# Performance work log

Hardware: AMD Instinct MI355X
Metric: run time of the kernel (lower is better)

The kernel has to match this reference:

```python
import jax, jax.numpy as jnp
import numpy as np

N_NODES = 50000
N_EDGES = 600000
D_IN = 128
D_HID = 128
N_CLASS = 40


def gcn_conv(x, edge_index, W, b, num_nodes):
    """PyG GCNConv: add self-loops, symmetric normalization, weight-then-propagate."""
    row, col = edge_index[0], edge_index[1]
    loop = jnp.arange(num_nodes)
    row = jnp.concatenate([row, loop])
    col = jnp.concatenate([col, loop])
    ew = jnp.ones(row.shape[0], dtype=x.dtype)
    deg = jax.ops.segment_sum(ew, col, num_segments=num_nodes)  # in-degree incl. self-loop
    dinv = jnp.where(deg > 0, jax.lax.rsqrt(deg), jnp.zeros((), x.dtype))
    norm = dinv[row] * dinv[col]  # [E+N]
    xw = x @ W  # [N, D]
    msg = norm[:, None] * xw[row]  # gather + scale, [E+N, D]
    out = jax.ops.segment_sum(msg, col, num_segments=num_nodes)  # scatter-add
    return out + b


def setup_inputs() -> dict:
    key = jax.random.key(0)
    ks = jax.random.split(key, 8)
    s_in = 1.0 / np.sqrt(D_IN)
    s_hid = 1.0 / np.sqrt(D_HID)
    return {
        "x": jax.random.normal(ks[0], (N_NODES, D_IN), jnp.float32),
        "edge_index": jax.random.randint(ks[1], (2, N_EDGES), 0, N_NODES, dtype=jnp.int64),
        "W_in": jax.random.normal(ks[2], (D_IN, D_HID), jnp.float32) * s_in,
        "b_in": jnp.zeros((D_HID,), jnp.float32),
        "W_gcn": jax.random.normal(ks[3], (D_HID, D_HID), jnp.float32) * s_hid,
        "b_gcn": jnp.zeros((D_HID,), jnp.float32),
        "W_cls": jax.random.normal(ks[4], (D_HID, N_CLASS), jnp.float32) * s_hid,
        "b_cls": jnp.zeros((N_CLASS,), jnp.float32),
    }


def reference(x, edge_index, W_in, b_in, W_gcn, b_gcn, W_cls, b_cls):
    h = jax.nn.relu(x @ W_in + b_in)               # linear_transform_in
    g = gcn_conv(h, edge_index, W_gcn, b_gcn, N_NODES)  # GCNConv
    y_hat = jax.nn.relu(g) @ W_cls + b_cls          # linear_cls_out
    return y_hat
```

## Files before the change

kernel.cpp:

```cpp
#include <hip/hip_runtime.h>


typedef __bf16 bf16x8 __attribute__((ext_vector_type(8)));
typedef float f32x4 __attribute__((ext_vector_type(4)));

#define NBUCK 512
#define CH_MAX 4704
#define PREP_BLKS 152

__device__ __forceinline__ ushort f2b(float f) {
  uint u = __float_as_uint(f);
  return (ushort)((u + 0x7FFFu + ((u >> 16) & 1u)) >> 16);
}
__device__ __forceinline__ float b2f_lo(uint u) { return __uint_as_float(u << 16); }
__device__ __forceinline__ float b2f_hi(uint u) { return __uint_as_float(u & 0xFFFF0000u); }

__device__ __forceinline__ void acc8s(float* a, uint4 v, float d) {
  a[0] = fmaf(d, b2f_lo(v.x), a[0]); a[1] = fmaf(d, b2f_hi(v.x), a[1]);
  a[2] = fmaf(d, b2f_lo(v.y), a[2]); a[3] = fmaf(d, b2f_hi(v.y), a[3]);
  a[4] = fmaf(d, b2f_lo(v.z), a[4]); a[5] = fmaf(d, b2f_hi(v.z), a[5]);
  a[6] = fmaf(d, b2f_lo(v.w), a[6]); a[7] = fmaf(d, b2f_hi(v.w), a[7]);
}

__global__ __launch_bounds__(256) void k_prep_chist(const float* __restrict__ Wi,
                                                    const float* __restrict__ Wg,
                                                    const float* __restrict__ Wc,
                                                    ushort* __restrict__ Ti,
                                                    ushort* __restrict__ Tg,
                                                    ushort* __restrict__ Tc,
                                                    const int* __restrict__ col,
                                                    int* __restrict__ H2,
                                                    int E, int chunk, int sortb) {
  __shared__ int hist[NBUCK];
  const int tid = threadIdx.x;
  if (blockIdx.x < PREP_BLKS) {
    int idx = blockIdx.x * 256 + tid;
    if (idx < 16384) {
      int c = idx >> 7, k = idx & 127;
      Ti[c * 128 + k] = f2b(Wi[k * 128 + c]);
    } else if (idx < 32768) {
      int j = idx - 16384;
      int c = j >> 7, k = j & 127;
      Tg[c * 128 + k] = f2b(Wg[k * 128 + c]);
    } else if (idx < 38912) {
      int j = idx - 32768;
      int c = j >> 7, k = j & 127;
      Tc[c * 128 + k] = (c < 40) ? f2b(Wc[k * 40 + c]) : (ushort)0;
    }
    return;
  }
  const int blk = blockIdx.x - PREP_BLKS;
  for (int b = tid; b < NBUCK; b += 256) hist[b] = 0;
  __syncthreads();
  const int e0 = blk * chunk;
  const int cnt = min(chunk, E - e0);
  for (int i = tid; i < cnt; i += 256)
    atomicAdd(&hist[((unsigned)col[e0 + i]) >> 7], 1);
  __syncthreads();
  for (int b = tid; b < NBUCK; b += 256)
    H2[b * sortb + blk] = hist[b];
}

__global__ __launch_bounds__(512) void k_scan_gemm1(const int* __restrict__ H2,
                                                    int* __restrict__ Hs,
                                                    int* __restrict__ cursor,
                                                    int sortb,
                                                    const float* __restrict__ x,
                                                    const ushort* __restrict__ Wti,
                                                    const float* __restrict__ b_in,
                                                    ushort* __restrict__ h, int nrows) {
  __shared__ __align__(16) char smem[69632];
  const int tid = threadIdx.x;
  if (blockIdx.x == 0) {
    int* sd = (int*)smem;
    int s = 0;
    const int4* p = (const int4*)&H2[tid * sortb];
    for (int j = 0; j < sortb / 4; ++j) { int4 v = p[j]; s += v.x + v.y + v.z + v.w; }
    sd[tid] = s;
    __syncthreads();
    for (int off = 1; off < 512; off <<= 1) {
      int u = (tid >= off) ? sd[tid - off] : 0;
      __syncthreads();
      sd[tid] += u;
      __syncthreads();
    }
    Hs[tid] = sd[tid] - s;
    if (tid == 511) Hs[NBUCK] = sd[511];
    cursor[tid] = 0;
    return;
  }
  ushort (*As)[136] = (ushort(*)[136])smem;
  ushort (*Bs)[136] = (ushort(*)[136])(smem + 128 * 136 * 2);
  const int row0 = (blockIdx.x - 1) * 128;
#pragma unroll
  for (int q = 0; q < 4; ++q) {
    int f = tid + 512 * q;
    int r = f >> 4, cw = f & 15;
    *(uint4*)&Bs[r][cw * 8] = *(const uint4*)&Wti[r * 128 + cw * 8];
  }
#pragma unroll
  for (int q = 0; q < 8; ++q) {
    int f = tid + 512 * q;
    int r = f >> 5, kc = f & 31;
    float4 v = make_float4(0.f, 0.f, 0.f, 0.f);
    if (row0 + r < nrows) v = *(const float4*)&x[(size_t)(row0 + r) * 128 + kc * 4];
    ushort4 o;
    o.x = f2b(v.x); o.y = f2b(v.y); o.z = f2b(v.z); o.w = f2b(v.w);
    *(ushort4*)&As[r][kc * 4] = o;
  }
  __syncthreads();

  const int wid = tid >> 6, lane = tid & 63;
  const int fr = lane & 15, fg = lane >> 4;
  f32x4 acc[8];
#pragma unroll
  for (int n = 0; n < 8; ++n) acc[n] = (f32x4){0.f, 0.f, 0.f, 0.f};
#pragma unroll
  for (int ks = 0; ks < 4; ++ks) {
    const int kb = ks * 32 + fg * 8;
    bf16x8 a = *(const bf16x8*)&As[wid * 16 + fr][kb];
#pragma unroll
    for (int n = 0; n < 8; ++n) {
      bf16x8 b = *(const bf16x8*)&Bs[n * 16 + fr][kb];
      acc[n] = __builtin_amdgcn_mfma_f32_16x16x32_bf16(a, b, acc[n], 0, 0, 0);
    }
  }
  const int r0 = row0 + wid * 16 + fg * 4;
#pragma unroll
  for (int n = 0; n < 8; ++n) {
    const int cn = n * 16 + fr;
    const float bv = b_in[cn];
#pragma unroll
    for (int i = 0; i < 4; ++i) {
      const int rr = r0 + i;
      if (rr < nrows) h[(size_t)rr * 128 + cn] = f2b(fmaxf(acc[n][i] + bv, 0.f));
    }
  }
}

__global__ __launch_bounds__(256) void k_reorder_gemm2(const int* __restrict__ row,
                                                       const int* __restrict__ col,
                                                       const int* __restrict__ Hs,
                                                       int* __restrict__ cursor,
                                                       uint* __restrict__ ebuf,
                                                       int E, int chunk, int sortb,
                                                       const ushort* __restrict__ h,
                                                       const ushort* __restrict__ Wtg,
                                                       ushort* __restrict__ xws,
                                                       int nrows) {
  __shared__ __align__(16) char smem[52224];
  const int tid = threadIdx.x;
  if (blockIdx.x < sortb) {
    int* hist   = (int*)smem;
    int* lstart = hist + NBUCK;
    int* cnt2   = lstart + NBUCK;
    int* obase  = cnt2 + NBUCK;
    uint* data  = (uint*)(obase + NBUCK);
    int* gpos   = (int*)(data + CH_MAX);
    int* sd     = gpos + CH_MAX;
    for (int b = tid; b < NBUCK; b += 256) { hist[b] = 0; cnt2[b] = 0; }
    __syncthreads();
    const int e0 = blockIdx.x * chunk;
    const int cnt = min(chunk, E - e0);
    for (int i = tid; i < cnt; i += 256)
      atomicAdd(&hist[((unsigned)col[e0 + i]) >> 7], 1);
    __syncthreads();
    const int h0 = hist[2 * tid], h1 = hist[2 * tid + 1];
    const int ps = h0 + h1;
    sd[tid] = ps;
    __syncthreads();
    for (int off = 1; off < 256; off <<= 1) {
      int u = (tid >= off) ? sd[tid - off] : 0;
      __syncthreads();
      sd[tid] += u;
      __syncthreads();
    }
    const int ex = sd[tid] - ps;
    lstart[2 * tid] = ex;
    lstart[2 * tid + 1] = ex + h0;
    obase[2 * tid]     = Hs[2 * tid]     + (h0 ? atomicAdd(&cursor[2 * tid], h0) : 0);
    obase[2 * tid + 1] = Hs[2 * tid + 1] + (h1 ? atomicAdd(&cursor[2 * tid + 1], h1) : 0);
    __syncthreads();
    for (int i = tid; i < cnt; i += 256) {
      const int c = col[e0 + i], r = row[e0 + i];
      const int b = ((unsigned)c) >> 7;
      const int rk = atomicAdd(&cnt2[b], 1);
      const int slot = lstart[b] + rk;
      data[slot] = ((uint)(c & 127) << 16) | (uint)r;
      gpos[slot] = obase[b] + rk;
    }
    __syncthreads();
    for (int i = tid; i < cnt; i += 256)
      ebuf[gpos[i]] = data[i];
    return;
  }
  ushort (*As)[136] = (ushort(*)[136])smem;
  ushort (*Bs)[136] = (ushort(*)[136])(smem + 64 * 136 * 2);
  const int row0 = (blockIdx.x - sortb) * 64;
#pragma unroll
  for (int q = 0; q < 8; ++q) {
    int f = tid + 256 * q;
    int r = f >> 4, cw = f & 15;
    *(uint4*)&Bs[r][cw * 8] = *(const uint4*)&Wtg[r * 128 + cw * 8];
  }
#pragma unroll
  for (int q = 0; q < 4; ++q) {
    int f = tid + 256 * q;
    int r = f >> 4, cw = f & 15;
    uint4 v = make_uint4(0u, 0u, 0u, 0u);
    if (row0 + r < nrows) v = *(const uint4*)&h[(size_t)(row0 + r) * 128 + cw * 8];
    *(uint4*)&As[r][cw * 8] = v;
  }
  __syncthreads();
  const int wid = tid >> 6, lane = tid & 63;
  const int fr = lane & 15, fg = lane >> 4;
  f32x4 acc[8];
#pragma unroll
  for (int n = 0; n < 8; ++n) acc[n] = (f32x4){0.f, 0.f, 0.f, 0.f};
#pragma unroll
  for (int ks = 0; ks < 4; ++ks) {
    const int kb = ks * 32 + fg * 8;
    bf16x8 a = *(const bf16x8*)&As[wid * 16 + fr][kb];
#pragma unroll
    for (int n = 0; n < 8; ++n) {
      bf16x8 b = *(const bf16x8*)&Bs[n * 16 + fr][kb];
      acc[n] = __builtin_amdgcn_mfma_f32_16x16x32_bf16(a, b, acc[n], 0, 0, 0);
    }
  }
  const int r0 = row0 + wid * 16 + fg * 4;
#pragma unroll
  for (int n = 0; n < 8; ++n) {
    const int cn = n * 16 + fr;
#pragma unroll
    for (int i = 0; i < 4; ++i) {
      const int rr = r0 + i;
      if (rr < nrows) xws[(size_t)rr * 128 + cn] = f2b(acc[n][i]);
    }
  }
}

__global__ __launch_bounds__(256) void k_sort2(const uint* __restrict__ ebuf,
                                               const int* __restrict__ Hs,
                                               int* __restrict__ srcrow,
                                               int* __restrict__ P,
                                               float* __restrict__ dinv,
                                               int n) {
  __shared__ int cnt[128];
  __shared__ int lstart[128];
  __shared__ int cnt2[128];
  __shared__ int sd[256];
  const int tid = threadIdx.x;
  if (tid < 128) { cnt[tid] = 0; cnt2[tid] = 0; }
  __syncthreads();
  const int b = blockIdx.x;
  const int start = Hs[b];
  const int end = Hs[b + 1];
  for (int i = start + tid; i < end; i += 256)
    atomicAdd(&cnt[ebuf[i] >> 16], 1);
  __syncthreads();
  const int cv = (tid < 128) ? cnt[tid] : 0;
  sd[tid] = cv;
  __syncthreads();
  for (int off = 1; off < 256; off <<= 1) {
    int u = (tid >= off) ? sd[tid - off] : 0;
    __syncthreads();
    sd[tid] += u;
    __syncthreads();
  }
  if (tid < 128) {
    const int ex = sd[tid] - cv;
    lstart[tid] = ex;
    const int node = b * 128 + tid;
    if (node < n) {
      P[node] = start + ex + cv;
      dinv[node] = rsqrtf((float)cv + 1.0f);
    }
  }
  __syncthreads();
  for (int i = start + tid; i < end; i += 256) {
    const uint v = ebuf[i];
    const int c = v >> 16;
    const int rk = atomicAdd(&cnt2[c], 1);
    srcrow[start + lstart[c] + rk] = (int)(v & 0xFFFFu);
  }
}

__global__ __launch_bounds__(512) void k_aggout(const int* __restrict__ P,
                                                const int* __restrict__ srcrow,
                                                const ushort* __restrict__ xws,
                                                const float* __restrict__ dinv,
                                                const float* __restrict__ b_gcn,
                                                const ushort* __restrict__ Wtc,
                                                const float* __restrict__ bc,
                                                float* __restrict__ out, int n) {
  __shared__ ushort ts[32][136];
  __shared__ ushort Bs[48][136];
  __shared__ int nextn;
  const int tid = threadIdx.x;
#pragma unroll
  for (int q = 0; q < 2; ++q) {
    int f = tid + 512 * q;
    if (f < 768) {
      int r = f >> 4, cw = f & 15;
      *(uint4*)&Bs[r][cw * 8] = *(const uint4*)&Wtc[r * 128 + cw * 8];
    }
  }
  if (tid == 0) nextn = 0;
  __syncthreads();

  const int wid = tid >> 6, lane = tid & 63;
  const int qt = lane >> 4, lq = lane & 15;
  const int row0 = blockIdx.x * 32;
  const size_t coff = (size_t)lq * 8;

  float bg[8];
#pragma unroll
  for (int j = 0; j < 8; ++j) bg[j] = b_gcn[lq * 8 + j];

  for (;;) {
    int idx;
    if (lane == 0) idx = atomicAdd(&nextn, 1);
    idx = __shfl(idx, 0);
    if (idx >= 32) break;
    const int c = row0 + idx;
    if (c < n) {
      const int begin = (c == 0) ? 0 : P[c - 1];
      const int end = P[c];
      float a[8];
#pragma unroll
      for (int j = 0; j < 8; ++j) a[j] = 0.f;
      int e = begin;
      for (; e + 8 <= end; e += 8) {
        const int r0 = srcrow[e + qt];
        const int r1 = srcrow[e + 4 + qt];
        const float d0 = dinv[r0], d1 = dinv[r1];
        const uint4 v0 = *(const uint4*)&xws[(size_t)r0 * 128 + coff];
        const uint4 v1 = *(const uint4*)&xws[(size_t)r1 * 128 + coff];
        acc8s(a, v0, d0);
        acc8s(a, v1, d1);
      }
      for (; e < end; e += 4) {
        if (e + qt < end) {
          const int r = srcrow[e + qt];
          const float d = dinv[r];
          const uint4 v = *(const uint4*)&xws[(size_t)r * 128 + coff];
          acc8s(a, v, d);
        }
      }
#pragma unroll
      for (int j = 0; j < 8; ++j) {
        a[j] += __shfl_xor(a[j], 16);
        a[j] += __shfl_xor(a[j], 32);
      }
      if (qt == 0) {
        const uint4 sv = *(const uint4*)&xws[(size_t)c * 128 + coff];
        const float dc = dinv[c];
        acc8s(a, sv, dc);
        const float t0 = fmaxf(fmaf(dc, a[0], bg[0]), 0.f);
        const float t1 = fmaxf(fmaf(dc, a[1], bg[1]), 0.f);
        const float t2 = fmaxf(fmaf(dc, a[2], bg[2]), 0.f);
        const float t3 = fmaxf(fmaf(dc, a[3], bg[3]), 0.f);
        const float t4 = fmaxf(fmaf(dc, a[4], bg[4]), 0.f);
        const float t5 = fmaxf(fmaf(dc, a[5], bg[5]), 0.f);
        const float t6 = fmaxf(fmaf(dc, a[6], bg[6]), 0.f);
        const float t7 = fmaxf(fmaf(dc, a[7], bg[7]), 0.f);
        uint4 o;
        o.x = ((uint)f2b(t1) << 16) | f2b(t0);
        o.y = ((uint)f2b(t3) << 16) | f2b(t2);
        o.z = ((uint)f2b(t5) << 16) | f2b(t4);
        o.w = ((uint)f2b(t7) << 16) | f2b(t6);
        *(uint4*)&ts[idx][coff] = o;
      }
    } else if (qt == 0) {
      *(uint4*)&ts[idx][coff] = make_uint4(0u, 0u, 0u, 0u);
    }
  }
  __syncthreads();

  if (wid < 6) {
    const int rb = wid & 1, nb = wid >> 1;
    const int fr = lane & 15, fg = lane >> 4;
    f32x4 acc = (f32x4){0.f, 0.f, 0.f, 0.f};
#pragma unroll
    for (int ks = 0; ks < 4; ++ks) {
      const int kb = ks * 32 + fg * 8;
      bf16x8 aa = *(const bf16x8*)&ts[rb * 16 + fr][kb];
      bf16x8 bb = *(const bf16x8*)&Bs[nb * 16 + fr][kb];
      acc = __builtin_amdgcn_mfma_f32_16x16x32_bf16(aa, bb, acc, 0, 0, 0);
    }
    const int cn = nb * 16 + fr;
    if (cn < 40) {
      const float bv = bc[cn];
      const int r0 = row0 + rb * 16 + fg * 4;
#pragma unroll
      for (int i = 0; i < 4; ++i) {
        const int rr = r0 + i;
        if (rr < n) out[(size_t)rr * 40 + cn] = acc[i] + bv;
      }
    }
  }
}

extern "C" void kernel_launch(void* const* d_in, const int* in_sizes, int n_in,
                              void* d_out, int out_size, void* d_ws, size_t ws_size,
                              hipStream_t stream) {
  const float* x     = (const float*)d_in[0];
  const int*   ei    = (const int*)d_in[1];
  const float* W_in  = (const float*)d_in[2];
  const float* b_in  = (const float*)d_in[3];
  const float* W_gcn = (const float*)d_in[4];
  const float* b_gcn = (const float*)d_in[5];
  const float* W_cls = (const float*)d_in[6];
  const float* b_cls = (const float*)d_in[7];
  float* out = (float*)d_out;

  const int N = in_sizes[0] / 128;
  const int E = in_sizes[1] / 2;
  const int* row = ei;
  const int* col = ei + E;

  const int sortb = (E + CH_MAX - 1) / CH_MAX;
  const int chunk = (E + sortb - 1) / sortb;
  const int nbuck = (N + 127) >> 7;

  ushort* h      = (ushort*)d_ws;
  ushort* xws    = h + (size_t)N * 128;
  ushort* Wti    = xws + (size_t)N * 128;
  ushort* Wtg    = Wti + 128 * 128;
  ushort* Wtc    = Wtg + 128 * 128;
  uint*   ebuf   = (uint*)(Wtc + 48 * 128);
  int*    srcrow = (int*)(ebuf + E);
  int*    H2     = srcrow + E;
  int*    Hs     = H2 + NBUCK * sortb;
  int*    cursor = Hs + NBUCK + 1;
  int*    P      = cursor + NBUCK;
  float*  dinv   = (float*)(P + N);

  k_prep_chist<<<PREP_BLKS + sortb, 256, 0, stream>>>(W_in, W_gcn, W_cls,
                                                      Wti, Wtg, Wtc,
                                                      col, H2, E, chunk, sortb);
  k_scan_gemm1<<<1 + (N + 127) / 128, 512, 0, stream>>>(H2, Hs, cursor, sortb,
                                                        x, Wti, b_in, h, N);
  k_reorder_gemm2<<<sortb + (N + 63) / 64, 256, 0, stream>>>(row, col, Hs, cursor,
                                                             ebuf, E, chunk, sortb,
                                                             h, Wtg, xws, N);
  k_sort2<<<nbuck, 256, 0, stream>>>(ebuf, Hs, srcrow, P, dinv, N);

  k_aggout<<<(N + 31) / 32, 512, 0, stream>>>(P, srcrow, xws, dinv, b_gcn,
                                              Wtc, b_cls, out, N);
}
```

Before: 89.55 us.

## Rebalance GEMM work across sort kernels and stage CSR indices in LDS

Splits the first GEMM across two launches and the second GEMM across the reorder and sort launches, so each kernel pairs sorting work with independent matmul tiles. All kernels move to 512-thread blocks sharing one templated GEMM tile routine. The aggregation kernel preloads the block's CSR offsets and source indices into shared memory when they fit. This adds complexity and more shared memory per block, which may lower occupancy in the sort and aggregation stages.

```diff
diff --git a/kernel.cpp b/kernel.cpp
--- a/kernel.cpp
+++ b/kernel.cpp
@@ -6,7 +6,8 @@
 
 #define NBUCK 512
 #define CH_MAX 4704
-#define PREP_BLKS 152
+#define PREP_BLKS 76
+#define SCAP 1024
 
 __device__ __forceinline__ ushort f2b(float f) {
   uint u = __float_as_uint(f);
@@ -22,19 +23,91 @@
   a[6] = fmaf(d, b2f_lo(v.w), a[6]); a[7] = fmaf(d, b2f_hi(v.w), a[7]);
 }
 
-__global__ __launch_bounds__(256) void k_prep_chist(const float* __restrict__ Wi,
-                                                    const float* __restrict__ Wg,
-                                                    const float* __restrict__ Wc,
-                                                    ushort* __restrict__ Ti,
-                                                    ushort* __restrict__ Tg,
-                                                    ushort* __restrict__ Tc,
-                                                    const int* __restrict__ col,
-                                                    int* __restrict__ H2,
-                                                    int E, int chunk, int sortb) {
+template<bool ABF16, bool RELU, bool BIAS>
+__device__ __forceinline__ void gemm_tile_512(const void* __restrict__ Ap,
+                                              const ushort* __restrict__ Wt,
+                                              const float* __restrict__ bias,
+                                              ushort* __restrict__ O,
+                                              int nrows, int row0,
+                                              char* smem, int tid) {
+  ushort (*As)[136] = (ushort(*)[136])smem;
+  ushort (*Bs)[136] = (ushort(*)[136])(smem + 128 * 136 * 2);
+#pragma unroll
+  for (int q = 0; q < 4; ++q) {
+    int f = tid + 512 * q;
+    int r = f >> 4, cw = f & 15;
+    *(uint4*)&Bs[r][cw * 8] = *(const uint4*)&Wt[r * 128 + cw * 8];
+  }
+  if (ABF16) {
+    const ushort* A = (const ushort*)Ap;
+#pragma unroll
+    for (int q = 0; q < 4; ++q) {
+      int f = tid + 512 * q;
+      int r = f >> 4, cw = f & 15;
+      uint4 v = make_uint4(0u, 0u, 0u, 0u);
+      if (row0 + r < nrows) v = *(const uint4*)&A[(size_t)(row0 + r) * 128 + cw * 8];
+      *(uint4*)&As[r][cw * 8] = v;
+    }
+  } else {
+    const float* A = (const float*)Ap;
+#pragma unroll
+    for (int q = 0; q < 8; ++q) {
+      int f = tid + 512 * q;
+      int r = f >> 5, kc = f & 31;
+      float4 v = make_float4(0.f, 0.f, 0.f, 0.f);
+      if (row0 + r < nrows) v = *(const float4*)&A[(size_t)(row0 + r) * 128 + kc * 4];
+      ushort4 o;
+      o.x = f2b(v.x); o.y = f2b(v.y); o.z = f2b(v.z); o.w = f2b(v.w);
+      *(ushort4*)&As[r][kc * 4] = o;
+    }
+  }
+  __syncthreads();
+
+  const int wid = tid >> 6, lane = tid & 63;
+  const int fr = lane & 15, fg = lane >> 4;
+  f32x4 acc[8];
+#pragma unroll
+  for (int nn = 0; nn < 8; ++nn) acc[nn] = (f32x4){0.f, 0.f, 0.f, 0.f};
+#pragma unroll
+  for (int ks = 0; ks < 4; ++ks) {
+    const int kb = ks * 32 + fg * 8;
+    bf16x8 a = *(const bf16x8*)&As[wid * 16 + fr][kb];
+#pragma unroll
+    for (int nn = 0; nn < 8; ++nn) {
+      bf16x8 b = *(const bf16x8*)&Bs[nn * 16 + fr][kb];
+      acc[nn] = __builtin_amdgcn_mfma_f32_16x16x32_bf16(a, b, acc[nn], 0, 0, 0);
+    }
+  }
+  const int r0 = row0 + wid * 16 + fg * 4;
+#pragma unroll
+  for (int nn = 0; nn < 8; ++nn) {
+    const int cn = nn * 16 + fr;
+    const float bv = BIAS ? bias[cn] : 0.f;
+#pragma unroll
+    for (int i = 0; i < 4; ++i) {
+      const int rr = r0 + i;
+      if (rr < nrows) {
+        float v = acc[nn][i] + bv;
+        if (RELU) v = fmaxf(v, 0.f);
+        O[(size_t)rr * 128 + cn] = f2b(v);
+      }
+    }
+  }
+}
+
+__global__ __launch_bounds__(512) void k_L1_prep_chist(const float* __restrict__ Wi,
+                                                       const float* __restrict__ Wg,
+                                                       const float* __restrict__ Wc,
+                                                       ushort* __restrict__ Ti,
+                                                       ushort* __restrict__ Tg,
+                                                       ushort* __restrict__ Tc,
+                                                       const int* __restrict__ col,
+                                                       int* __restrict__ H2,
+                                                       int E, int chunk, int sortb) {
   __shared__ int hist[NBUCK];
   const int tid = threadIdx.x;
   if (blockIdx.x < PREP_BLKS) {
-    int idx = blockIdx.x * 256 + tid;
+    int idx = blockIdx.x * 512 + tid;
     if (idx < 16384) {
       int c = idx >> 7, k = idx & 127;
       Ti[c * 128 + k] = f2b(Wi[k * 128 + c]);
@@ -50,25 +123,24 @@
     return;
   }
   const int blk = blockIdx.x - PREP_BLKS;
-  for (int b = tid; b < NBUCK; b += 256) hist[b] = 0;
+  if (tid < NBUCK) hist[tid] = 0;
   __syncthreads();
   const int e0 = blk * chunk;
   const int cnt = min(chunk, E - e0);
-  for (int i = tid; i < cnt; i += 256)
+  for (int i = tid; i < cnt; i += 512)
     atomicAdd(&hist[((unsigned)col[e0 + i]) >> 7], 1);
   __syncthreads();
-  for (int b = tid; b < NBUCK; b += 256)
-    H2[b * sortb + blk] = hist[b];
-}
-
-__global__ __launch_bounds__(512) void k_scan_gemm1(const int* __restrict__ H2,
-                                                    int* __restrict__ Hs,
-                                                    int* __restrict__ cursor,
-                                                    int sortb,
-                                                    const float* __restrict__ x,
-                                                    const ushort* __restrict__ Wti,
-                                                    const float* __restrict__ b_in,
-                                                    ushort* __restrict__ h, int nrows) {
+  if (tid < NBUCK) H2[tid * sortb + blk] = hist[tid];
+}
+
+__global__ __launch_bounds__(512) void k_L2_scan_g1a(const int* __restrict__ H2,
+                                                     int* __restrict__ Hs,
+                                                     int* __restrict__ cursor,
+                                                     int sortb,
+                                                     const float* __restrict__ x,
+                                                     const ushort* __restrict__ Wti,
+                                                     const float* __restrict__ b_in,
+                                                     ushort* __restrict__ h, int nrows) {
   __shared__ __align__(16) char smem[69632];
   const int tid = threadIdx.x;
   if (blockIdx.x == 0) {
@@ -89,68 +161,28 @@
     cursor[tid] = 0;
     return;
   }
-  ushort (*As)[136] = (ushort(*)[136])smem;
-  ushort (*Bs)[136] = (ushort(*)[136])(smem + 128 * 136 * 2);
-  const int row0 = (blockIdx.x - 1) * 128;
-#pragma unroll
-  for (int q = 0; q < 4; ++q) {
-    int f = tid + 512 * q;
-    int r = f >> 4, cw = f & 15;
-    *(uint4*)&Bs[r][cw * 8] = *(const uint4*)&Wti[r * 128 + cw * 8];
-  }
-#pragma unroll
-  for (int q = 0; q < 8; ++q) {
-    int f = tid + 512 * q;
-    int r = f >> 5, kc = f & 31;
-    float4 v = make_float4(0.f, 0.f, 0.f, 0.f);
-    if (row0 + r < nrows) v = *(const float4*)&x[(size_t)(row0 + r) * 128 + kc * 4];
-    ushort4 o;
-    o.x = f2b(v.x); o.y = f2b(v.y); o.z = f2b(v.z); o.w = f2b(v.w);
-    *(ushort4*)&As[r][kc * 4] = o;
-  }
-  __syncthreads();
-
-  const int wid = tid >> 6, lane = tid & 63;
-  const int fr = lane & 15, fg = lane >> 4;
-  f32x4 acc[8];
-#pragma unroll
-  for (int n = 0; n < 8; ++n) acc[n] = (f32x4){0.f, 0.f, 0.f, 0.f};
-#pragma unroll
-  for (int ks = 0; ks < 4; ++ks) {
-    const int kb = ks * 32 + fg * 8;
-    bf16x8 a = *(const bf16x8*)&As[wid * 16 + fr][kb];
-#pragma unroll
-    for (int n = 0; n < 8; ++n) {
-      bf16x8 b = *(const bf16x8*)&Bs[n * 16 + fr][kb];
-      acc[n] = __builtin_amdgcn_mfma_f32_16x16x32_bf16(a, b, acc[n], 0, 0, 0);
-    }
-  }
-  const int r0 = row0 + wid * 16 + fg * 4;
-#pragma unroll
-  for (int n = 0; n < 8; ++n) {
-    const int cn = n * 16 + fr;
-    const float bv = b_in[cn];
-#pragma unroll
-    for (int i = 0; i < 4; ++i) {
-      const int rr = r0 + i;
-      if (rr < nrows) h[(size_t)rr * 128 + cn] = f2b(fmaxf(acc[n][i] + bv, 0.f));
-    }
-  }
-}
-
-__global__ __launch_bounds__(256) void k_reorder_gemm2(const int* __restrict__ row,
-                                                       const int* __restrict__ col,
-                                                       const int* __restrict__ Hs,
-                                                       int* __restrict__ cursor,
-                                                       uint* __restrict__ ebuf,
-                                                       int E, int chunk, int sortb,
-                                                       const ushort* __restrict__ h,
-                                                       const ushort* __restrict__ Wtg,
-                                                       ushort* __restrict__ xws,
-                                                       int nrows) {
-  __shared__ __align__(16) char smem[52224];
+  gemm_tile_512<false, true, true>(x, Wti, b_in, h, nrows,
+                                   (blockIdx.x - 1) * 128, smem, tid);
+}
+
+__global__ __launch_bounds__(512) void k_L3_reorder_g1b_g2a(const int* __restrict__ row,
+                                                            const int* __restrict__ col,
+                                                            const int* __restrict__ Hs,
+                                                            int* __restrict__ cursor,
+                                                            uint* __restrict__ ebuf,
+                                                            int E, int chunk, int sortb,
+                                                            const float* __restrict__ x,
+                                                            const ushort* __restrict__ Wti,
+                                                            const float* __restrict__ b_in,
+                                                            const ushort* __restrict__ Wtg,
+                                                            ushort* __restrict__ h,
+                                                            ushort* __restrict__ xws,
+                                                            int nrows) {
+  __shared__ __align__(16) char smem[69632];
   const int tid = threadIdx.x;
-  if (blockIdx.x < sortb) {
+  const int NT = (nrows + 127) >> 7;
+  const int SPLIT = (NT + 1) >> 1;
+  if (blockIdx.x < (unsigned)sortb) {
     int* hist   = (int*)smem;
     int* lstart = hist + NBUCK;
     int* cnt2   = lstart + NBUCK;
@@ -158,30 +190,26 @@
     uint* data  = (uint*)(obase + NBUCK);
     int* gpos   = (int*)(data + CH_MAX);
     int* sd     = gpos + CH_MAX;
-    for (int b = tid; b < NBUCK; b += 256) { hist[b] = 0; cnt2[b] = 0; }
+    hist[tid] = 0; cnt2[tid] = 0;
     __syncthreads();
     const int e0 = blockIdx.x * chunk;
     const int cnt = min(chunk, E - e0);
-    for (int i = tid; i < cnt; i += 256)
+    for (int i = tid; i < cnt; i += 512)
       atomicAdd(&hist[((unsigned)col[e0 + i]) >> 7], 1);
     __syncthreads();
-    const int h0 = hist[2 * tid], h1 = hist[2 * tid + 1];
-    const int ps = h0 + h1;
-    sd[tid] = ps;
-    __syncthreads();
-    for (int off = 1; off < 256; off <<= 1) {
+    const int h0 = hist[tid];
+    sd[tid] = h0;
+    __syncthreads();
+    for (int off = 1; off < 512; off <<= 1) {
       int u = (tid >= off) ? sd[tid - off] : 0;
       __syncthreads();
       sd[tid] += u;
       __syncthreads();
     }
-    const int ex = sd[tid] - ps;
-    lstart[2 * tid] = ex;
-    lstart[2 * tid + 1] = ex + h0;
-    obase[2 * tid]     = Hs[2 * tid]     + (h0 ? atomicAdd(&cursor[2 * tid], h0) : 0);
-    obase[2 * tid + 1] = Hs[2 * tid + 1] + (h1 ? atomicAdd(&cursor[2 * tid + 1], h1) : 0);
-    __syncthreads();
-    for (int i = tid; i < cnt; i += 256) {
+    lstart[tid] = sd[tid] - h0;
+    obase[tid] = Hs[tid] + (h0 ? atomicAdd(&cursor[tid], h0) : 0);
+    __syncthreads();
+    for (int i = tid; i < cnt; i += 512) {
       const int c = col[e0 + i], r = row[e0 + i];
       const int b = ((unsigned)c) >> 7;
       const int rk = atomicAdd(&cnt2[b], 1);
@@ -190,99 +218,77 @@
       gpos[slot] = obase[b] + rk;
     }
     __syncthreads();
-    for (int i = tid; i < cnt; i += 256)
+    for (int i = tid; i < cnt; i += 512)
       ebuf[gpos[i]] = data[i];
     return;
   }
-  ushort (*As)[136] = (ushort(*)[136])smem;
-  ushort (*Bs)[136] = (ushort(*)[136])(smem + 64 * 136 * 2);
-  const int row0 = (blockIdx.x - sortb) * 64;
-#pragma unroll
-  for (int q = 0; q < 8; ++q) {
-    int f = tid + 256 * q;
-    int r = f >> 4, cw = f & 15;
-    *(uint4*)&Bs[r][cw * 8] = *(const uint4*)&Wtg[r * 128 + cw * 8];
-  }
-#pragma unroll
-  for (int q = 0; q < 4; ++q) {
-    int f = tid + 256 * q;
-    int r = f >> 4, cw = f & 15;
-    uint4 v = make_uint4(0u, 0u, 0u, 0u);
-    if (row0 + r < nrows) v = *(const uint4*)&h[(size_t)(row0 + r) * 128 + cw * 8];
-    *(uint4*)&As[r][cw * 8] = v;
-  }
-  __syncthreads();
-  const int wid = tid >> 6, lane = tid & 63;
-  const int fr = lane & 15, fg = lane >> 4;
-  f32x4 acc[8];
-#pragma unroll
-  for (int n = 0; n < 8; ++n) acc[n] = (f32x4){0.f, 0.f, 0.f, 0.f};
-#pragma unroll
-  for (int ks = 0; ks < 4; ++ks) {
-    const int kb = ks * 32 + fg * 8;
-    bf16x8 a = *(const bf16x8*)&As[wid * 16 + fr][kb];
-#pragma unroll
-    for (int n = 0; n < 8; ++n) {
-      bf16x8 b = *(const bf16x8*)&Bs[n * 16 + fr][kb];
-      acc[n] = __builtin_amdgcn_mfma_f32_16x16x32_bf16(a, b, acc[n], 0, 0, 0);
-    }
-  }
-  const int r0 = row0 + wid * 16 + fg * 4;
-#pragma unroll
-  for (int n = 0; n < 8; ++n) {
-    const int cn = n * 16 + fr;
-#pragma unroll
-    for (int i = 0; i < 4; ++i) {
-      const int rr = r0 + i;
-      if (rr < nrows) xws[(size_t)rr * 128 + cn] = f2b(acc[n][i]);
-    }
-  }
-}
-
-__global__ __launch_bounds__(256) void k_sort2(const uint* __restrict__ ebuf,
-                                               const int* __restrict__ Hs,
-                                               int* __restrict__ srcrow,
-                                               int* __restrict__ P,
-                                               float* __restrict__ dinv,
-                                               int n) {
-  __shared__ int cnt[128];
-  __shared__ int lstart[128];
-  __shared__ int cnt2[128];
-  __shared__ int sd[256];
+  const int t = blockIdx.x - sortb;
+  if (t < NT - SPLIT) {
+    gemm_tile_512<false, true, true>(x, Wti, b_in, h, nrows,
+                                     (SPLIT + t) * 128, smem, tid);
+  } else {
+    gemm_tile_512<true, false, false>(h, Wtg, nullptr, xws, nrows,
+                                      (t - (NT - SPLIT)) * 128, smem, tid);
+  }
+}
+
+__global__ __launch_bounds__(512) void k_L4_sort_g2b(const uint* __restrict__ ebuf,
+                                                     const int* __restrict__ Hs,
+                                                     int* __restrict__ srcrow,
+                                                     int* __restrict__ P,
+                                                     float* __restrict__ dinv,
+                                                     int nbuck,
+                                                     const ushort* __restrict__ h,
+                                                     const ushort* __restrict__ Wtg,
+                                                     ushort* __restrict__ xws,
+                                                     int n) {
+  __shared__ __align__(16) char smem[69632];
   const int tid = threadIdx.x;
-  if (tid < 128) { cnt[tid] = 0; cnt2[tid] = 0; }
-  __syncthreads();
-  const int b = blockIdx.x;
-  const int start = Hs[b];
-  const int end = Hs[b + 1];
-  for (int i = start + tid; i < end; i += 256)
-    atomicAdd(&cnt[ebuf[i] >> 16], 1);
-  __syncthreads();
-  const int cv = (tid < 128) ? cnt[tid] : 0;
-  sd[tid] = cv;
-  __syncthreads();
-  for (int off = 1; off < 256; off <<= 1) {
-    int u = (tid >= off) ? sd[tid - off] : 0;
-    __syncthreads();
-    sd[tid] += u;
-    __syncthreads();
-  }
-  if (tid < 128) {
-    const int ex = sd[tid] - cv;
-    lstart[tid] = ex;
-    const int node = b * 128 + tid;
-    if (node < n) {
-      P[node] = start + ex + cv;
-      dinv[node] = rsqrtf((float)cv + 1.0f);
-    }
-  }
-  __syncthreads();
-  for (int i = start + tid; i < end; i += 256) {
-    const uint v = ebuf[i];
-    const int c = v >> 16;
-    const int rk = atomicAdd(&cnt2[c], 1);
-    srcrow[start + lstart[c] + rk] = (int)(v & 0xFFFFu);
-  }
+  if (blockIdx.x < (unsigned)nbuck) {
+    int* cnt    = (int*)smem;
+    int* lstart = cnt + 128;
+    int* cnt2   = lstart + 128;
+    int* sd     = cnt2 + 128;
+    if (tid < 128) { cnt[tid] = 0; cnt2[tid] = 0; }
+    __syncthreads();
+    const int b = blockIdx.x;
+    const int start = Hs[b];
+    const int end = Hs[b + 1];
+    for (int i = start + tid; i < end; i += 512)
+      atomicAdd(&cnt[ebuf[i] >> 16], 1);
+    __syncthreads();
+    const int cv = (tid < 128) ? cnt[tid] : 0;
+    sd[tid] = cv;
+    __syncthreads();
+    for (int off = 1; off < 128; off <<= 1) {
+      int u = (tid >= off) ? sd[tid - off] : 0;
+      __syncthreads();
+      sd[tid] += u;
+      __syncthreads();
+    }
+    if (tid < 128) {
+      const int ex = sd[tid] - cv;
+      lstart[tid] = ex;
+      const int node = b * 128 + tid;
+      if (node < n) {
+        P[node] = start + ex + cv;
+        dinv[node] = rsqrtf((float)cv + 1.0f);
+      }
+    }
+    __syncthreads();
+    for (int i = start + tid; i < end; i += 512) {
+      const uint v = ebuf[i];
+      const int c = v >> 16;
+      const int rk = atomicAdd(&cnt2[c], 1);
+      srcrow[start + lstart[c] + rk] = (int)(v & 0xFFFFu);
+    }
+    return;
+  }
+  const int NT = (n + 127) >> 7;
+  const int SPLIT = (NT + 1) >> 1;
+  const int t = blockIdx.x - nbuck;
+  gemm_tile_512<true, false, false>(h, Wtg, nullptr, xws, n,
+                                    (SPLIT + t) * 128, smem, tid);
 }
 
 __global__ __launch_bounds__(512) void k_aggout(const int* __restrict__ P,
@@ -295,8 +301,11 @@
                                                 float* __restrict__ out, int n) {
   __shared__ ushort ts[32][136];
   __shared__ ushort Bs[48][136];
+  __shared__ int eLds[SCAP];
+  __shared__ int pb[33];
   __shared__ int nextn;
   const int tid = threadIdx.x;
+  const int row0 = blockIdx.x * 32;
 #pragma unroll
   for (int q = 0; q < 2; ++q) {
     int f = tid + 512 * q;
@@ -305,12 +314,22 @@
       *(uint4*)&Bs[r][cw * 8] = *(const uint4*)&Wtc[r * 128 + cw * 8];
     }
   }
+  if (tid < 33) {
+    int node = row0 + tid - 1;
+    pb[tid] = (node < 0) ? 0 : P[node < n ? node : (n - 1)];
+  }
   if (tid == 0) nextn = 0;
+  __syncthreads();
+  const int sStart = pb[0];
+  const int tot = pb[32] - sStart;
+  const bool inL = (tot <= SCAP);
+  if (inL) {
+    for (int i = tid; i < tot; i += 512) eLds[i] = srcrow[sStart + i];
+  }
   __syncthreads();
 
   const int wid = tid >> 6, lane = tid & 63;
   const int qt = lane >> 4, lq = lane & 15;
-  const int row0 = blockIdx.x * 32;
   const size_t coff = (size_t)lq * 8;
 
   float bg[8];
@@ -324,27 +343,49 @@
     if (idx >= 32) break;
     const int c = row0 + idx;
     if (c < n) {
-      const int begin = (c == 0) ? 0 : P[c - 1];
-      const int end = P[c];
+      const int len = pb[idx + 1] - pb[idx];
       float a[8];
 #pragma unroll
       for (int j = 0; j < 8; ++j) a[j] = 0.f;
-      int e = begin;
-      for (; e + 8 <= end; e += 8) {
-        const int r0 = srcrow[e + qt];
-        const int r1 = srcrow[e + 4 + qt];
-        const float d0 = dinv[r0], d1 = dinv[r1];
-        const uint4 v0 = *(const uint4*)&xws[(size_t)r0 * 128 + coff];
-        const uint4 v1 = *(const uint4*)&xws[(size_t)r1 * 128 + coff];
-        acc8s(a, v0, d0);
-        acc8s(a, v1, d1);
-      }
-      for (; e < end; e += 4) {
-        if (e + qt < end) {
-          const int r = srcrow[e + qt];
-          const float d = dinv[r];
-          const uint4 v = *(const uint4*)&xws[(size_t)r * 128 + coff];
-          acc8s(a, v, d);
+      if (inL) {
+        const int base = pb[idx] - sStart;
+        int e = 0;
+        for (; e + 8 <= len; e += 8) {
+          const int r0 = eLds[base + e + qt];
+          const int r1 = eLds[base + e + 4 + qt];
+          const float d0 = dinv[r0], d1 = dinv[r1];
+          const uint4 v0 = *(const uint4*)&xws[(size_t)r0 * 128 + coff];
+          const uint4 v1 = *(const uint4*)&xws[(size_t)r1 * 128 + coff];
+          acc8s(a, v0, d0);
+          acc8s(a, v1, d1);
+        }
+        for (; e < len; e += 4) {
+          if (e + qt < len) {
+            const int r = eLds[base + e + qt];
+            const float d = dinv[r];
+            const uint4 v = *(const uint4*)&xws[(size_t)r * 128 + coff];
+            acc8s(a, v, d);
+          }
+        }
+      } else {
+        const int base = pb[idx];
+        int e = 0;
+        for (; e + 8 <= len; e += 8) {
+          const int r0 = srcrow[base + e + qt];
+          const int r1 = srcrow[base + e + 4 + qt];
+          const float d0 = dinv[r0], d1 = dinv[r1];
+          const uint4 v0 = *(const uint4*)&xws[(size_t)r0 * 128 + coff];
+          const uint4 v1 = *(const uint4*)&xws[(size_t)r1 * 128 + coff];
+          acc8s(a, v0, d0);
+          acc8s(a, v1, d1);
+        }
+        for (; e < len; e += 4) {
+          if (e + qt < len) {
+            const int r = srcrow[base + e + qt];
+            const float d = dinv[r];
+            const uint4 v = *(const uint4*)&xws[(size_t)r * 128 + coff];
+            acc8s(a, v, d);
+          }
         }
       }
 #pragma unroll
@@ -422,6 +463,8 @@
   const int sortb = (E + CH_MAX - 1) / CH_MAX;
   const int chunk = (E + sortb - 1) / sortb;
   const int nbuck = (N + 127) >> 7;
+  const int NT    = (N + 127) >> 7;
+  const int SPLIT = (NT + 1) >> 1;
 
   ushort* h      = (ushort*)d_ws;
   ushort* xws    = h + (size_t)N * 128;
@@ -436,16 +479,19 @@
   int*    P      = cursor + NBUCK;
   float*  dinv   = (float*)(P + N);
 
-  k_prep_chist<<<PREP_BLKS + sortb, 256, 0, stream>>>(W_in, W_gcn, W_cls,
-                                                      Wti, Wtg, Wtc,
-                                                      col, H2, E, chunk, sortb);
-  k_scan_gemm1<<<1 + (N + 127) / 128, 512, 0, stream>>>(H2, Hs, cursor, sortb,
-                                                        x, Wti, b_in, h, N);
-  k_reorder_gemm2<<<sortb + (N + 63) / 64, 256, 0, stream>>>(row, col, Hs, cursor,
-                                                             ebuf, E, chunk, sortb,
-                                                             h, Wtg, xws, N);
-  k_sort2<<<nbuck, 256, 0, stream>>>(ebuf, Hs, srcrow, P, dinv, N);
-
-  k_aggout<<<(N + 31) / 32, 512, 0, stream>>>(P, srcrow, xws, dinv, b_gcn,
-                                              Wtc, b_cls, out, N);
-}
+  k_L1_prep_chist<<<PREP_BLKS + sortb, 512, 0, stream>>>(
+      W_in, W_gcn, W_cls, Wti, Wtg, Wtc, col, H2, E, chunk, sortb);
+
+  k_L2_scan_g1a<<<1 + SPLIT, 512, 0, stream>>>(
+      H2, Hs, cursor, sortb, x, Wti, b_in, h, N);
+
+  k_L3_reorder_g1b_g2a<<<sortb + (NT - SPLIT) + SPLIT, 512, 0, stream>>>(
+      row, col, Hs, cursor, ebuf, E, chunk, sortb,
+      x, Wti, b_in, Wtg, h, xws, N);
+
+  k_L4_sort_g2b<<<nbuck + (NT - SPLIT), 512, 0, stream>>>(
+      ebuf, Hs, srcrow, P, dinv, nbuck, h, Wtg, xws, N);
+
+  k_aggout<<<(N + 31) / 32, 512, 0, stream>>>(
+      P, srcrow, xws, dinv, b_gcn, Wtc, b_cls, out, N);
+}
```

Measured after the change: 79.64 us. -11.1%, faster.
